# Kernel optimization log

Hardware: AMD Instinct MI355X
Metric: run time of the kernel (lower is better)

The kernel has to match this reference:

```python
import jax, jax.numpy as jnp
import numpy as np

B, S, D, F, E, K = 2, 2048, 1024, 4096, 8, 2


def setup_inputs() -> dict:
    key = jax.random.key(0)
    ks = jax.random.split(key, 6)
    s = 0.02  # init scale
    return {
        "x": jax.random.normal(ks[0], (B, S, D), dtype=jnp.float32),
        "Wr": jax.random.normal(ks[1], (D, E), dtype=jnp.float32) * s,
        "br": jnp.zeros((E,), dtype=jnp.float32),
        "W1": jax.random.normal(ks[2], (E, D, F), dtype=jnp.float32) * s,
        "b1": jnp.zeros((E, F), dtype=jnp.float32),
        "W2": jax.random.normal(ks[3], (E, F, D), dtype=jnp.float32) * s,
        "b2": jnp.zeros((E, D), dtype=jnp.float32),
        "top_k": K,
    }


def reference(x, Wr, br, W1, b1, W2, b2, top_k):
    b, s, d = x.shape
    e = Wr.shape[1]
    xt = x.reshape(-1, d)                              # [T, D], T = b*s
    logits = xt @ Wr + br                              # [T, E]
    probs = jax.nn.softmax(logits, axis=-1)            # [T, E] router probabilities
    topw, topi = jax.lax.top_k(probs, top_k)           # [T, K] each
    # combine weight per (token, expert): weight if expert in token's top-k else 0
    cw = jnp.sum(jax.nn.one_hot(topi, e, dtype=x.dtype) * topw[..., None], axis=1)  # [T, E]
    # dense grouped FFN: every expert over every token, then weighted combine
    h = jax.nn.relu(jnp.einsum('td,edf->tef', xt, W1) + b1)   # [T, E, F]
    y = jnp.einsum('tef,efd->ted', h, W2) + b2                # [T, E, D]
    out = jnp.einsum('te,ted->td', cw, y).reshape(b, s, d)    # [B, S, D]
    return out, probs.reshape(b, s, e)
```

## Files before the change

kernel.cpp:

```cpp
#include <hip/hip_runtime.h>
#include <hip/hip_bf16.h>


#define T_TOK 4096
#define D_DIM 1024
#define F_DIM 4096
#define E_NUM 8
#define CAP_ROWS 9216
#define N_TILES (CAP_ROWS/128)

typedef __attribute__((ext_vector_type(8))) short short8v;
typedef __attribute__((ext_vector_type(8))) unsigned short ushort8v;
typedef __attribute__((ext_vector_type(4))) float f32x4;

static __device__ __forceinline__ unsigned short f2bf(float f){
  union { float f; unsigned u; } v; v.f = f;
  unsigned r = (v.u + 0x7fffu + ((v.u >> 16) & 1u)) >> 16;
  return (unsigned short)r;
}
static __device__ __forceinline__ float bf2f(unsigned short s){
  union { unsigned u; float f; } v; v.u = ((unsigned)s) << 16;
  return v.f;
}

static __device__ __forceinline__ void gload16(const void* g, void* l) {
  __builtin_amdgcn_global_load_lds(
      (const __attribute__((address_space(1))) unsigned int*)g,
      (__attribute__((address_space(3))) unsigned int*)l, 16, 0, 0);
}

__global__ __launch_bounds__(256) void k_fused0(
    const float* __restrict__ x, const float* __restrict__ Wr,
    const float* __restrict__ br, float* __restrict__ probs_out,
    int* __restrict__ topi, float* __restrict__ topw, int* __restrict__ counts,
    unsigned short* __restrict__ xbf,
    const float* __restrict__ W1, unsigned short* __restrict__ W1t)
{
  __shared__ unsigned short ls[64][66];
  const int b = blockIdx.x;
  if (b < T_TOK/4) {
    const int lane = threadIdx.x & 63;
    const int t = b * 4 + (threadIdx.x >> 6);
    float xv[16];
    #pragma unroll
    for (int i = 0; i < 16; ++i) xv[i] = x[(size_t)t*D_DIM + i*64 + lane];
    #pragma unroll
    for (int i = 0; i < 16; ++i) xbf[(size_t)t*D_DIM + i*64 + lane] = f2bf(xv[i]);
    float pe[E_NUM];
    #pragma unroll
    for (int e = 0; e < E_NUM; ++e) {
      float p = 0.f;
      #pragma unroll
      for (int i = 0; i < 16; ++i) p += xv[i] * Wr[(i*64 + lane)*E_NUM + e];
      #pragma unroll
      for (int off = 32; off >= 1; off >>= 1) p += __shfl_xor(p, off);
      pe[e] = p + br[e];
    }
    float m = pe[0];
    #pragma unroll
    for (int e = 1; e < E_NUM; ++e) m = fmaxf(m, pe[e]);
    float s = 0.f;
    #pragma unroll
    for (int e = 0; e < E_NUM; ++e) { pe[e] = expf(pe[e] - m); s += pe[e]; }
    const float inv = 1.f / s;
    int e1 = 0; float v1 = pe[0];
    #pragma unroll
    for (int e = 1; e < E_NUM; ++e) if (pe[e] > v1) { v1 = pe[e]; e1 = e; }
    int e2 = (e1 == 0) ? 1 : 0; float v2 = pe[e2];
    #pragma unroll
    for (int e = 0; e < E_NUM; ++e) if (e != e1 && pe[e] > v2) { v2 = pe[e]; e2 = e; }
    if (lane == 0) {
      #pragma unroll
      for (int e = 0; e < E_NUM; ++e) probs_out[(size_t)t*E_NUM + e] = pe[e] * inv;
      topi[t*2+0] = e1; topw[t*2+0] = v1 * inv;
      topi[t*2+1] = e2; topw[t*2+1] = v2 * inv;
      atomicAdd(&counts[e1], 1);
      atomicAdd(&counts[e2], 1);
    }
  } else {
    const int tb = b - T_TOK/4;
    const int e = tb >> 7;
    const int rem = tb & 127;
    const int c0 = (rem >> 1) * 64;
    const int rg = (rem & 1) * 512;
    const size_t eo = (size_t)e * D_DIM * F_DIM;
    const int t = threadIdx.x;
    const int rr = t >> 4, cc = (t & 15) * 4;
    const int kc = (t & 7) * 8, nn0 = t >> 3;
    for (int s = 0; s < 8; ++s) {
      const int r0 = rg + s * 64;
      #pragma unroll
      for (int p = 0; p < 4; ++p) {
        const float4 v = *(const float4*)&W1[eo + (size_t)(r0 + p*16 + rr)*F_DIM + c0 + cc];
        ls[p*16+rr][cc+0]=f2bf(v.x); ls[p*16+rr][cc+1]=f2bf(v.y);
        ls[p*16+rr][cc+2]=f2bf(v.z); ls[p*16+rr][cc+3]=f2bf(v.w);
      }
      __syncthreads();
      #pragma unroll
      for (int p = 0; p < 2; ++p) {
        const int nn = nn0 + p*32;
        ushort8v o;
        #pragma unroll
        for (int j = 0; j < 8; ++j) o[j] = ls[kc + j][nn];
        *(ushort8v*)&W1t[eo + (size_t)(c0 + nn)*D_DIM + r0 + kc] = o;
      }
      __syncthreads();
    }
  }
}

__global__ __launch_bounds__(256) void k_assign(
    const int* __restrict__ counts,
    const int* __restrict__ topi, const float* __restrict__ topw,
    int* __restrict__ cursor,
    int* __restrict__ rows_token, float* __restrict__ rows_w,
    int* __restrict__ pair_of, int* __restrict__ tile_e)
{
  __shared__ int base_s[E_NUM + 1];
  if (threadIdx.x == 0) {
    int base = 0;
    #pragma unroll
    for (int e = 0; e < E_NUM; ++e) {
      base_s[e] = base;
      base += ((counts[e] + 127) >> 7) << 7;
    }
    base_s[E_NUM] = base;
  }
  __syncthreads();
  if (blockIdx.x == 0 && threadIdx.x < N_TILES) {
    const int r0 = threadIdx.x << 7;
    int e = -1;
    #pragma unroll
    for (int k = 0; k < E_NUM; ++k)
      if (r0 >= base_s[k] && r0 < base_s[k+1]) e = k;
    tile_e[threadIdx.x] = e;
  }
  const int t = blockIdx.x * 256 + threadIdx.x;
  if (t < T_TOK) {
    #pragma unroll
    for (int k = 0; k < 2; ++k) {
      const int e = topi[t*2+k];
      const int slot = atomicAdd(&cursor[e], 1);
      const int pid = base_s[e] + slot;
      rows_token[pid] = t;
      rows_w[pid] = topw[t*2+k];
      pair_of[t*2+k] = pid;
    }
  }
}

template<int R, int C>
__global__ __launch_bounds__(256) void k_tcvt(const float* __restrict__ in,
                                              unsigned short* __restrict__ out)
{
  const size_t eo = (size_t)blockIdx.z * R * C;
  const int r0 = blockIdx.y * 64, c0 = blockIdx.x * 64;
  __shared__ unsigned short ls[64][66];
  const int t = threadIdx.x;
  const int rr = t >> 4, cc = (t & 15) * 4;
  #pragma unroll
  for (int p = 0; p < 4; ++p) {
    const float4 v = *(const float4*)&in[eo + (size_t)(r0 + p*16 + rr)*C + c0 + cc];
    ls[p*16+rr][cc+0]=f2bf(v.x); ls[p*16+rr][cc+1]=f2bf(v.y);
    ls[p*16+rr][cc+2]=f2bf(v.z); ls[p*16+rr][cc+3]=f2bf(v.w);
  }
  __syncthreads();
  const int kc = (t & 7) * 8, nn0 = t >> 3;
  #pragma unroll
  for (int p = 0; p < 2; ++p) {
    const int nn = nn0 + p*32;
    ushort8v o;
    #pragma unroll
    for (int j = 0; j < 8; ++j) o[j] = ls[kc + j][nn];
    *(ushort8v*)&out[eo + (size_t)(c0 + nn)*R + r0 + kc] = o;
  }
}

template<bool GATHER, int NDIM, int KFULL, int EPI>
static __device__ __forceinline__ void gemm_tile(
    const unsigned short* __restrict__ A,
    const unsigned short* __restrict__ Bt,
    const float* __restrict__ bias,
    const int* __restrict__ tile_e,
    const int* __restrict__ rows_token,
    const float* __restrict__ rows_w,
    unsigned short* __restrict__ outp,
    int bx, int by, int z, int nkt, int kch,
    unsigned short (*LB)[256*64])
{
  const int e = tile_e[by];
  if (e < 0) return;
  const int rt = by * 128;
  const int ntc = bx * 128;
  const int koff = z * kch;
  const int tid = threadIdx.x;
  const int lane = tid & 63;
  const int w = tid >> 6;
  const int lr = lane >> 3;
  const int g  = (lane & 7) ^ lr;
  const unsigned short* gp[8];
  unsigned lbase[8];
  if (w < 2) {
    #pragma unroll
    for (int i = 0; i < 8; ++i) {
      const int rl = w*64 + i*8 + lr;
      const int rowidx = GATHER ? rows_token[rt + rl] : (rt + rl);
      gp[i] = A + (size_t)rowidx * KFULL + koff + g*8;
      lbase[i] = (unsigned)((w*64 + i*8) * 64);
    }
  } else {
    const unsigned short* Be = Bt + (size_t)e * NDIM * KFULL;
    #pragma unroll
    for (int i = 0; i < 8; ++i) {
      const int rl = (w-2)*64 + i*8 + lr;
      gp[i] = Be + (size_t)(ntc + rl) * KFULL + koff + g*8;
      lbase[i] = (unsigned)((128*64) + ((w-2)*64 + i*8) * 64);
    }
  }
  const int wr = w >> 1, wc = w & 1;
  const int cl = lane & 15, rgb = lane >> 4;
  const int sz = cl & 7;
  f32x4 acc[4][4] = {};

  #define STG8(tt, bb)                                          \
    { const int _ko = (tt) * 64;                                \
      _Pragma("unroll")                                         \
      for (int _i = 0; _i < 8; ++_i)                            \
        gload16(gp[_i] + _ko, &LB[bb][lbase[_i]]); }

  STG8(0, 0)
  asm volatile("s_waitcnt vmcnt(0)" ::: "memory");
  __builtin_amdgcn_s_barrier();

  for (int t = 0; t < nkt; ++t) {
    const int bb = t & 1;
    if (t + 1 < nkt) STG8(t+1, bb^1)
    const unsigned short* Sb = &LB[bb][0];
    short8v a[4][2], b[4][2];
    #pragma unroll
    for (int m = 0; m < 4; ++m) {
      a[m][0] = *(const short8v*)&Sb[(wr*64 + m*16 + cl)*64 + ((0*4+rgb)^sz)*8];
      a[m][1] = *(const short8v*)&Sb[(wr*64 + m*16 + cl)*64 + ((1*4+rgb)^sz)*8];
    }
    #pragma unroll
    for (int n = 0; n < 4; ++n) {
      b[n][0] = *(const short8v*)&Sb[(128*64) + (wc*64 + n*16 + cl)*64 + ((0*4+rgb)^sz)*8];
      b[n][1] = *(const short8v*)&Sb[(128*64) + (wc*64 + n*16 + cl)*64 + ((1*4+rgb)^sz)*8];
    }
    __builtin_amdgcn_s_setprio(1);
    #pragma unroll
    for (int m = 0; m < 4; ++m)
      #pragma unroll
      for (int n = 0; n < 4; ++n) {
        acc[m][n] = __builtin_amdgcn_mfma_f32_16x16x32_bf16(a[m][0], b[n][0], acc[m][n], 0, 0, 0);
        acc[m][n] = __builtin_amdgcn_mfma_f32_16x16x32_bf16(a[m][1], b[n][1], acc[m][n], 0, 0, 0);
      }
    __builtin_amdgcn_s_setprio(0);
    asm volatile("s_waitcnt vmcnt(0)" ::: "memory");
    __builtin_amdgcn_s_barrier();
  }
  #undef STG8

  unsigned short* op = outp;
  if (EPI == 2) op += (size_t)z * CAP_ROWS * NDIM;
  const bool addb = (EPI == 1) || (z == 0);
  const size_t ebias = (size_t)e * NDIM;
  #pragma unroll
  for (int m = 0; m < 4; ++m) {
    const int row = rt + wr*64 + m*16 + rgb*4;
    float4 rw4 = make_float4(0,0,0,0);
    if (EPI == 2) rw4 = *(const float4*)&rows_w[row];
    #pragma unroll
    for (int n = 0; n < 4; ++n) {
      const int col = ntc + wc*64 + n*16 + cl;
      const float bv = addb ? bias[ebias + col] : 0.f;
      #pragma unroll
      for (int r = 0; r < 4; ++r) {
        float v = acc[m][n][r] + bv;
        if (EPI == 1) v = fmaxf(v, 0.f);
        else          v *= ((const float*)&rw4)[r];
        const unsigned short hb = f2bf(v);
        const unsigned short ob = (unsigned short)__shfl_xor((int)(unsigned)hb, 1);
        if ((lane & 1) == 0) {
          const unsigned pk = (unsigned)hb | ((unsigned)ob << 16);
          *(unsigned*)&op[(size_t)(row + r)*NDIM + col] = pk;
        }
      }
    }
  }
}

template<bool GATHER, int NDIM, int KFULL, int EPI>
__global__ __launch_bounds__(256, 2) void k_gemm(
    const unsigned short* __restrict__ A,
    const unsigned short* __restrict__ Bt,
    const float* __restrict__ bias,
    const int* __restrict__ tile_e,
    const int* __restrict__ rows_token,
    const float* __restrict__ rows_w,
    unsigned short* __restrict__ outp,
    int nkt, int kch)
{
  __shared__ __align__(16) unsigned short LB[2][256 * 64];
  const int tot = gridDim.x * gridDim.y;
  int flat = blockIdx.x * gridDim.y + blockIdx.y;
  flat = (flat & 7) * (tot >> 3) + (flat >> 3);
  gemm_tile<GATHER, NDIM, KFULL, EPI>(A, Bt, bias, tile_e, rows_token, rows_w,
                                      outp, flat / gridDim.y, flat % gridDim.y,
                                      blockIdx.z, nkt, kch, LB);
}

__global__ __launch_bounds__(256, 2) void k_fused1(
    const unsigned short* __restrict__ xbf,
    const unsigned short* __restrict__ W1t,
    const float* __restrict__ b1,
    const int* __restrict__ tile_e,
    const int* __restrict__ rows_token,
    const float* __restrict__ rows_w,
    unsigned short* __restrict__ h,
    const float* __restrict__ W2,
    unsigned short* __restrict__ W2t)
{
  __shared__ __align__(16) unsigned short LB[2][256 * 64];
  constexpr int NG = (F_DIM/128) * N_TILES;
  const int b = blockIdx.x;
  if (b < NG) {
    const int x = b & 31;
    const int y = b >> 5;
    int flat = x * N_TILES + y;
    flat = (flat & 7) * (NG >> 3) + (flat >> 3);
    gemm_tile<true, F_DIM, D_DIM, 1>(xbf, W1t, b1, tile_e, rows_token, rows_w,
                                     h, flat / N_TILES, flat % N_TILES, 0,
                                     D_DIM/64, D_DIM, LB);
  } else {
    auto ls = (unsigned short (*)[66])(&LB[0][0]);
    const int tb = b - NG;
    const int e = tb >> 7;
    const int rem = tb & 127;
    const int c0 = (rem & 15) * 64;
    const int rg = (rem >> 4) * 512;
    const size_t eo = (size_t)e * F_DIM * D_DIM;
    const int t = threadIdx.x;
    const int rr = t >> 4, cc = (t & 15) * 4;
    const int kc = (t & 7) * 8, nn0 = t >> 3;
    for (int s = 0; s < 8; ++s) {
      const int r0 = rg + s * 64;
      #pragma unroll
      for (int p = 0; p < 4; ++p) {
        const float4 v = *(const float4*)&W2[eo + (size_t)(r0 + p*16 + rr)*D_DIM + c0 + cc];
        ls[p*16+rr][cc+0]=f2bf(v.x); ls[p*16+rr][cc+1]=f2bf(v.y);
        ls[p*16+rr][cc+2]=f2bf(v.z); ls[p*16+rr][cc+3]=f2bf(v.w);
      }
      __syncthreads();
      #pragma unroll
      for (int p = 0; p < 2; ++p) {
        const int nn = nn0 + p*32;
        ushort8v o;
        #pragma unroll
        for (int j = 0; j < 8; ++j) o[j] = ls[kc + j][nn];
        *(ushort8v*)&W2t[eo + (size_t)(c0 + nn)*F_DIM + r0 + kc] = o;
      }
      __syncthreads();
    }
  }
}

__global__ __launch_bounds__(256) void k_combine(
    const unsigned short* __restrict__ yp, const int* __restrict__ pair_of,
    float* __restrict__ out, int ksplit)
{
  const int gid = blockIdx.x * 256 + threadIdx.x;
  const int t = gid >> 7;
  const int c = (gid & 127) * 8;
  float o[8] = {0,0,0,0,0,0,0,0};
  #pragma unroll
  for (int k = 0; k < 2; ++k) {
    const int p = pair_of[t*2+k];
    for (int s = 0; s < ksplit; ++s) {
      const ushort8v v = *(const ushort8v*)&yp[((size_t)s*CAP_ROWS + p)*D_DIM + c];
      #pragma unroll
      for (int j = 0; j < 8; ++j) o[j] += bf2f(v[j]);
    }
  }
  float4 o0; o0.x=o[0]; o0.y=o[1]; o0.z=o[2]; o0.w=o[3];
  float4 o1; o1.x=o[4]; o1.y=o[5]; o1.z=o[6]; o1.w=o[7];
  *(float4*)&out[(size_t)t*D_DIM + c]     = o0;
  *(float4*)&out[(size_t)t*D_DIM + c + 4] = o1;
}

extern "C" void kernel_launch(void* const* d_in, const int* in_sizes, int n_in,
                              void* d_out, int out_size, void* d_ws, size_t ws_size,
                              hipStream_t stream)
{
  const float* x  = (const float*)d_in[0];
  const float* Wr = (const float*)d_in[1];
  const float* br = (const float*)d_in[2];
  const float* W1 = (const float*)d_in[3];
  const float* b1 = (const float*)d_in[4];
  const float* W2 = (const float*)d_in[5];
  const float* b2 = (const float*)d_in[6];
  (void)in_sizes; (void)n_in; (void)out_size;

  float* out   = (float*)d_out;
  float* probs = out + (size_t)T_TOK * D_DIM;

  char* w = (char*)d_ws;
  size_t off = 0;
  int*   counts     = (int*)(w + off); off += 256;
  int*   cursor     = (int*)(w + off); off += 256;
  int*   rows_token = (int*)(w + off); off += (size_t)CAP_ROWS*4;
  float* rows_w     = (float*)(w + off); off += (size_t)CAP_ROWS*4;
  const size_t zbytes = off;
  int*   tile_e     = (int*)(w + off); off += 3072;
  int*   topi       = (int*)(w + off); off += (size_t)T_TOK*2*4;
  float* topw       = (float*)(w + off); off += (size_t)T_TOK*2*4;
  int*   pair_of    = (int*)(w + off); off += (size_t)T_TOK*2*4;
  off = (off + 255) & ~(size_t)255;
  unsigned short* xbf = (unsigned short*)(w + off); off += (size_t)T_TOK*D_DIM*2;
  unsigned short* W1t = (unsigned short*)(w + off); off += (size_t)E_NUM*D_DIM*F_DIM*2;

  const size_t WT = (size_t)E_NUM*D_DIM*F_DIM*2;
  const size_t HB = (size_t)CAP_ROWS*F_DIM*2;
  const size_t YP = (size_t)CAP_ROWS*D_DIM*2;

  bool fused; int ksplit;
  if      (ws_size >= off + WT + HB + 4*YP) { fused = true;  ksplit = 4; }
  else if (ws_size >= off + WT + HB + 2*YP) { fused = true;  ksplit = 2; }
  else if (ws_size >= off + HB + 4*YP)      { fused = false; ksplit = 4; }
  else if (ws_size >= off + HB + 2*YP)      { fused = false; ksplit = 2; }
  else                                      { fused = false; ksplit = 1; }

  unsigned short* W2t;
  unsigned short* h;
  if (fused) {
    W2t = (unsigned short*)(w + off); off += WT;
    h   = (unsigned short*)(w + off); off += HB;
  } else {
    W2t = W1t;
    h   = (unsigned short*)(w + off); off += HB;
  }
  unsigned short* yp = (unsigned short*)(w + off);
  const int kch2 = F_DIM / ksplit;
  const int nkt2 = kch2 / 64;

  hipMemsetAsync(d_ws, 0, zbytes, stream);
  k_fused0<<<T_TOK/4 + 1024, 256, 0, stream>>>(
      x, Wr, br, probs, topi, topw, counts, xbf, W1, W1t);
  k_assign<<<T_TOK / 256, 256, 0, stream>>>(counts, topi, topw, cursor,
                                            rows_token, rows_w, pair_of, tile_e);
  if (fused) {
    k_fused1<<<(F_DIM/128)*N_TILES + 1024, 256, 0, stream>>>(
        xbf, W1t, b1, tile_e, rows_token, rows_w, h, W2, W2t);
  } else {
    k_gemm<true, F_DIM, D_DIM, 1><<<dim3(F_DIM/128, N_TILES), 256, 0, stream>>>(
        xbf, W1t, b1, tile_e, rows_token, rows_w, h, D_DIM/64, D_DIM);
    k_tcvt<F_DIM, D_DIM><<<dim3(D_DIM/64, F_DIM/64, E_NUM), 256, 0, stream>>>(W2, W2t);
  }
  k_gemm<false, D_DIM, F_DIM, 2><<<dim3(D_DIM/128, N_TILES, ksplit), 256, 0, stream>>>(
      h, W2t, b2, tile_e, rows_token, rows_w, yp, nkt2, kch2);
  k_combine<<<T_TOK * D_DIM / 8 / 256, 256, 0, stream>>>(yp, pair_of, out, ksplit);
}
```

Baseline: 439.5 us.

## Fold token-to-expert assignment into router kernel via last-block ticket; allow split-K 8

Result: slower. 582.6 us (+32.6%).

```diff
diff --git a/kernel.cpp b/kernel.cpp
--- a/kernel.cpp
+++ b/kernel.cpp
@@ -34,7 +34,10 @@
     const float* __restrict__ br, float* __restrict__ probs_out,
     int* __restrict__ topi, float* __restrict__ topw, int* __restrict__ counts,
     unsigned short* __restrict__ xbf,
-    const float* __restrict__ W1, unsigned short* __restrict__ W1t)
+    const float* __restrict__ W1, unsigned short* __restrict__ W1t,
+    int* __restrict__ done, int* __restrict__ cursor,
+    int* __restrict__ rows_token, float* __restrict__ rows_w,
+    int* __restrict__ pair_of, int* __restrict__ tile_e)
 {
   __shared__ unsigned short ls[64][66];
   const int b = blockIdx.x;
@@ -76,6 +79,45 @@
       topi[t*2+1] = e2; topw[t*2+1] = v2 * inv;
       atomicAdd(&counts[e1], 1);
       atomicAdd(&counts[e2], 1);
+    }
+    __syncthreads();
+    __threadfence();
+    __syncthreads();
+    __shared__ int ticket_s;
+    if (threadIdx.x == 0) ticket_s = atomicAdd(done, 1);
+    __syncthreads();
+    if (ticket_s == T_TOK/4 - 1) {
+      __threadfence();
+      __shared__ int base_s[E_NUM + 1];
+      if (threadIdx.x == 0) {
+        int base = 0;
+        #pragma unroll
+        for (int e = 0; e < E_NUM; ++e) {
+          base_s[e] = base;
+          base += ((counts[e] + 127) >> 7) << 7;
+        }
+        base_s[E_NUM] = base;
+      }
+      __syncthreads();
+      if (threadIdx.x < N_TILES) {
+        const int r0 = threadIdx.x << 7;
+        int e = -1;
+        #pragma unroll
+        for (int k = 0; k < E_NUM; ++k)
+          if (r0 >= base_s[k] && r0 < base_s[k+1]) e = k;
+        tile_e[threadIdx.x] = e;
+      }
+      for (int tt = threadIdx.x; tt < T_TOK; tt += 256) {
+        #pragma unroll
+        for (int k = 0; k < 2; ++k) {
+          const int e = topi[tt*2+k];
+          const int slot = atomicAdd(&cursor[e], 1);
+          const int pid = base_s[e] + slot;
+          rows_token[pid] = tt;
+          rows_w[pid] = topw[tt*2+k];
+          pair_of[tt*2+k] = pid;
+        }
+      }
     }
   } else {
     const int tb = b - T_TOK/4;
@@ -105,46 +147,6 @@
         *(ushort8v*)&W1t[eo + (size_t)(c0 + nn)*D_DIM + r0 + kc] = o;
       }
       __syncthreads();
-    }
-  }
-}
-
-__global__ __launch_bounds__(256) void k_assign(
-    const int* __restrict__ counts,
-    const int* __restrict__ topi, const float* __restrict__ topw,
-    int* __restrict__ cursor,
-    int* __restrict__ rows_token, float* __restrict__ rows_w,
-    int* __restrict__ pair_of, int* __restrict__ tile_e)
-{
-  __shared__ int base_s[E_NUM + 1];
-  if (threadIdx.x == 0) {
-    int base = 0;
-    #pragma unroll
-    for (int e = 0; e < E_NUM; ++e) {
-      base_s[e] = base;
-      base += ((counts[e] + 127) >> 7) << 7;
-    }
-    base_s[E_NUM] = base;
-  }
-  __syncthreads();
-  if (blockIdx.x == 0 && threadIdx.x < N_TILES) {
-    const int r0 = threadIdx.x << 7;
-    int e = -1;
-    #pragma unroll
-    for (int k = 0; k < E_NUM; ++k)
-      if (r0 >= base_s[k] && r0 < base_s[k+1]) e = k;
-    tile_e[threadIdx.x] = e;
-  }
-  const int t = blockIdx.x * 256 + threadIdx.x;
-  if (t < T_TOK) {
-    #pragma unroll
-    for (int k = 0; k < 2; ++k) {
-      const int e = topi[t*2+k];
-      const int slot = atomicAdd(&cursor[e], 1);
-      const int pid = base_s[e] + slot;
-      rows_token[pid] = t;
-      rows_w[pid] = topw[t*2+k];
-      pair_of[t*2+k] = pid;
     }
   }
 }
@@ -408,6 +410,7 @@
   size_t off = 0;
   int*   counts     = (int*)(w + off); off += 256;
   int*   cursor     = (int*)(w + off); off += 256;
+  int*   done       = (int*)(w + off); off += 256;
   int*   rows_token = (int*)(w + off); off += (size_t)CAP_ROWS*4;
   float* rows_w     = (float*)(w + off); off += (size_t)CAP_ROWS*4;
   const size_t zbytes = off;
@@ -424,7 +427,8 @@
   const size_t YP = (size_t)CAP_ROWS*D_DIM*2;
 
   bool fused; int ksplit;
-  if      (ws_size >= off + WT + HB + 4*YP) { fused = true;  ksplit = 4; }
+  if      (ws_size >= off + WT + HB + 8*YP) { fused = true;  ksplit = 8; }
+  else if (ws_size >= off + WT + HB + 4*YP) { fused = true;  ksplit = 4; }
   else if (ws_size >= off + WT + HB + 2*YP) { fused = true;  ksplit = 2; }
   else if (ws_size >= off + HB + 4*YP)      { fused = false; ksplit = 4; }
   else if (ws_size >= off + HB + 2*YP)      { fused = false; ksplit = 2; }
@@ -445,9 +449,8 @@
 
   hipMemsetAsync(d_ws, 0, zbytes, stream);
   k_fused0<<<T_TOK/4 + 1024, 256, 0, stream>>>(
-      x, Wr, br, probs, topi, topw, counts, xbf, W1, W1t);
-  k_assign<<<T_TOK / 256, 256, 0, stream>>>(counts, topi, topw, cursor,
-                                            rows_token, rows_w, pair_of, tile_e);
+      x, Wr, br, probs, topi, topw, counts, xbf, W1, W1t,
+      done, cursor, rows_token, rows_w, pair_of, tile_e);
   if (fused) {
     k_fused1<<<(F_DIM/128)*N_TILES + 1024, 256, 0, stream>>>(
         xbf, W1t, b1, tile_e, rows_token, rows_w, h, W2, W2t);
```
